# Kernel tuning notes

Measured on AMD Instinct MI355X. Metric: run time of the kernel, lower is better.

Reference implementation:

```python
import jax, jax.numpy as jnp
import numpy as np

HIDDEN = 256
N_HEADS = 4
HEAD_DIM = HIDDEN // N_HEADS
SCALE = float(np.sqrt(HEAD_DIM))


def setup_inputs() -> dict:
    key = jax.random.key(0)
    ks = jax.random.split(key, 10)
    B, NQ, NKV = 2, 4096, 4096
    s = 1.0 / np.sqrt(HIDDEN)
    inp = {
        "query": jax.random.normal(ks[0], (B, NQ, HIDDEN), dtype=jnp.float32),
        "key_value": jax.random.normal(ks[1], (B, NKV, HIDDEN), dtype=jnp.float32),
        "kv_mask": jnp.ones((B, NKV), dtype=jnp.int32),
        "Wq": jax.random.uniform(ks[2], (HIDDEN, HIDDEN), jnp.float32, -s, s),
        "bq": jnp.zeros((HIDDEN,), jnp.float32),
        "Wk": jax.random.uniform(ks[3], (HIDDEN, HIDDEN), jnp.float32, -s, s),
        "bk": jnp.zeros((HIDDEN,), jnp.float32),
        "Wv": jax.random.uniform(ks[4], (HIDDEN, HIDDEN), jnp.float32, -s, s),
        "bv": jnp.zeros((HIDDEN,), jnp.float32),
        "Wo": jax.random.uniform(ks[5], (HIDDEN, HIDDEN), jnp.float32, -s, s),
        "bo": jnp.zeros((HIDDEN,), jnp.float32),
    }
    return inp


def reference(query, key_value, kv_mask, Wq, bq, Wk, bk, Wv, bv, Wo, bo):
    B, NQ, D = query.shape
    NKV = key_value.shape[1]
    # projections; reshape to (B, H, S, Dh)
    q = (query @ Wq + bq).reshape(B, NQ, N_HEADS, HEAD_DIM).transpose(0, 2, 1, 3)
    k = (key_value @ Wk + bk).reshape(B, NKV, N_HEADS, HEAD_DIM).transpose(0, 2, 1, 3)
    v = (key_value @ Wv + bv).reshape(B, NKV, N_HEADS, HEAD_DIM).transpose(0, 2, 1, 3)
    # scores: (B, H, NQ, NKV)
    attn = jnp.einsum("bhqd,bhkd->bhqk", q, k) / SCALE
    mask = (kv_mask != 0)[:, None, None, :]  # (B,1,1,NKV)
    attn = jnp.where(mask, attn, -jnp.inf)
    attn = jax.nn.softmax(attn, axis=-1)
    # dropout is identity in eval mode (reference is deterministic)
    out = jnp.einsum("bhqk,bhkd->bhqd", attn, v)
    out = out.transpose(0, 2, 1, 3).reshape(B, NQ, D)
    return out @ Wo + bo
```

## Files before the change

kernel.cpp:

```cpp
#include <hip/hip_runtime.h>
#include <hip/hip_bf16.h>
#include <math.h>

#define HID   256
#define NHEADS  4
#define HDIM   64
#define SEQ  4096
#define BATCH   2
#define MTOK (BATCH * SEQ)
#define LOG2E 1.44269504088896340736f
#define MFIX  8.0f

typedef short bf16x8 __attribute__((ext_vector_type(8)));
typedef float f32x4  __attribute__((ext_vector_type(4)));

__device__ __forceinline__ unsigned short f2b(float f) {
  union { float f; unsigned u; } v; v.f = f;
  return (unsigned short)((v.u + 0x7FFFu + ((v.u >> 16) & 1u)) >> 16);
}
__device__ __forceinline__ unsigned pkb(float a, float b) {
  __hip_bfloat162 h = __float22bfloat162_rn(make_float2(a, b));
  union { __hip_bfloat162 h; unsigned u; } v; v.h = h;
  return v.u;
}
__device__ __forceinline__ float exp2_(float x) {
#if __has_builtin(__builtin_amdgcn_exp2f)
  return __builtin_amdgcn_exp2f(x);
#else
  return exp2f(x);
#endif
}

__global__ __launch_bounds__(256)
void cast_wt(const float* __restrict__ W0, const float* __restrict__ W1,
             const float* __restrict__ W2, const float* __restrict__ W3,
             unsigned short* __restrict__ Wt) {
  __shared__ float t[64][65];
  const float* Ws[4] = {W0, W1, W2, W3};
  const float scl[4] = {0.125f * LOG2E, 1.f, 1.f, 1.f};
  const int wsel = blockIdx.y;
  const float* W = Ws[wsel];
  const float s = scl[wsel];
  unsigned short* O = Wt + (size_t)wsel * HID * HID;
  const int kt = (blockIdx.x & 3) * 64, nt = (blockIdx.x >> 2) * 64;
  const int tid = threadIdx.x;
#pragma unroll
  for (int p = 0; p < 4; ++p) {
    int i = p * 256 + tid;
    int r = i >> 4, c4 = (i & 15) * 4;
    *(float4*)&t[r][c4] = *(const float4*)&W[(size_t)(kt + r) * HID + nt + c4];
  }
  __syncthreads();
#pragma unroll
  for (int p = 0; p < 4; ++p) {
    int i = p * 256 + tid;
    int rn = i >> 4, ck = (i & 15) * 4;
    ushort4 o;
    o.x = f2b(t[ck + 0][rn] * s);
    o.y = f2b(t[ck + 1][rn] * s);
    o.z = f2b(t[ck + 2][rn] * s);
    o.w = f2b(t[ck + 3][rn] * s);
    *(ushort4*)&O[(size_t)(nt + rn) * HID + kt + ck] = o;
  }
}

__global__ __launch_bounds__(256)
void gemm_qkv(const float* __restrict__ query, const float* __restrict__ keyv,
              const unsigned short* __restrict__ wts,
              const float* __restrict__ bq, const float* __restrict__ bk,
              const float* __restrict__ bv,
              unsigned short* qp, unsigned short* kp, unsigned short* vtp) {
  __shared__ __align__(16) unsigned short As[2][64][136];
  __shared__ __align__(16) unsigned short Bs[64][136];
  float (*L)[68] = (float (*)[68])&Bs[0][0];

  const int tid = threadIdx.x;
  const int w = tid >> 6, lane = tid & 63, lq = lane & 15, quad = lane >> 4;
  const int wm = w & 1, wn = w >> 1;
  const int z = blockIdx.y;
  const int m0 = blockIdx.x * 64;

  const float* A = (z == 0) ? query : keyv;
  const unsigned short* Bt = wts + (size_t)z * HID * HID;
  const float* bias = (z == 0) ? bq : ((z == 1) ? bk : bv);
  const float bscale = (z == 0) ? 0.125f * LOG2E : 1.0f;

#pragma unroll
  for (int p = 0; p < 16; ++p) {
    int i = p * 256 + tid;
    int r = i >> 6, c4 = (i & 63) * 4;
    float4 f4 = *(const float4*)&A[(size_t)(m0 + r) * HID + c4];
    unsigned lo = pkb(f4.x, f4.y), hi = pkb(f4.z, f4.w);
    *(uint2*)&As[c4 >> 7][r][c4 & 127] = make_uint2(lo, hi);
  }
  __syncthreads();

  for (int n = 0; n < 4; ++n) {
    const int n0 = n * 64;
    f32x4 acc[2][2];
#pragma unroll
    for (int i = 0; i < 2; ++i)
#pragma unroll
      for (int j = 0; j < 2; ++j) acc[i][j] = (f32x4){0.f, 0.f, 0.f, 0.f};

#pragma unroll
    for (int kt = 0; kt < 2; ++kt) {
#pragma unroll
      for (int p = 0; p < 4; ++p) {
        int i = p * 256 + tid;
        int r = i >> 4, c8 = (i & 15) * 8;
        *(uint4*)&Bs[r][c8] =
            *(const uint4*)&Bt[(size_t)(n0 + r) * HID + kt * 128 + c8];
      }
      __syncthreads();
#pragma unroll
      for (int ks = 0; ks < 4; ++ks) {
        bf16x8 a0 = *(const bf16x8*)&As[kt][wm * 32 + lq][ks * 32 + quad * 8];
        bf16x8 a1 = *(const bf16x8*)&As[kt][wm * 32 + 16 + lq][ks * 32 + quad * 8];
        bf16x8 b0 = *(const bf16x8*)&Bs[wn * 32 + lq][ks * 32 + quad * 8];
        bf16x8 b1 = *(const bf16x8*)&Bs[wn * 32 + 16 + lq][ks * 32 + quad * 8];
        acc[0][0] = __builtin_amdgcn_mfma_f32_16x16x32_bf16(a0, b0, acc[0][0], 0, 0, 0);
        acc[0][1] = __builtin_amdgcn_mfma_f32_16x16x32_bf16(a0, b1, acc[0][1], 0, 0, 0);
        acc[1][0] = __builtin_amdgcn_mfma_f32_16x16x32_bf16(a1, b0, acc[1][0], 0, 0, 0);
        acc[1][1] = __builtin_amdgcn_mfma_f32_16x16x32_bf16(a1, b1, acc[1][1], 0, 0, 0);
      }
      __syncthreads();
    }

#pragma unroll
    for (int ni = 0; ni < 2; ++ni) {
      const float bv = bias[n0 + wn * 32 + ni * 16 + lq] * bscale;
#pragma unroll
      for (int mi = 0; mi < 2; ++mi)
#pragma unroll
        for (int r = 0; r < 4; ++r)
          L[wm * 32 + mi * 16 + quad * 4 + r][wn * 32 + ni * 16 + lq] =
              acc[mi][ni][r] + bv;
    }
    __syncthreads();

    if (z == 2) {
      const int nn = tid >> 2, mb4 = (tid & 3) * 16;
      __align__(16) unsigned short tmp[16];
#pragma unroll
      for (int j = 0; j < 16; ++j) {
        int p = mb4 + j;
        int k = ((p & 3) << 4) + (p >> 2);
        tmp[j] = f2b(L[k][nn]);
      }
      *(uint4*)&vtp[(size_t)(n0 + nn) * MTOK + m0 + mb4]     = *(uint4*)&tmp[0];
      *(uint4*)&vtp[(size_t)(n0 + nn) * MTOK + m0 + mb4 + 8] = *(uint4*)&tmp[8];
    } else {
      unsigned short* Y = (z == 0) ? qp : kp;
      const int r = tid >> 2, cb = (tid & 3) * 16;
      __align__(16) unsigned short tmp[16];
#pragma unroll
      for (int j = 0; j < 4; ++j) {
        float4 v4 = *(const float4*)&L[r][cb + j * 4];
        *(uint2*)&tmp[j * 4] = make_uint2(pkb(v4.x, v4.y), pkb(v4.z, v4.w));
      }
      *(uint4*)&Y[(size_t)(m0 + r) * HID + n0 + cb]     = *(uint4*)&tmp[0];
      *(uint4*)&Y[(size_t)(m0 + r) * HID + n0 + cb + 8] = *(uint4*)&tmp[8];
    }
    __syncthreads();
  }
}

__global__ __launch_bounds__(256)
void gemm_out(const unsigned short* __restrict__ ao,
              const unsigned short* __restrict__ wot,
              const float* __restrict__ bo, float* __restrict__ out) {
  __shared__ __align__(16) unsigned short As[64][136];
  __shared__ __align__(16) unsigned short Bs[64][136];
  float (*L)[68] = (float (*)[68])&As[0][0];

  const int tid = threadIdx.x;
  const int w = tid >> 6, lane = tid & 63, lq = lane & 15, quad = lane >> 4;
  const int wm = w & 1, wn = w >> 1;
  const int m0 = blockIdx.y * 64, n0 = blockIdx.x * 64;

  f32x4 acc[2][2];
#pragma unroll
  for (int i = 0; i < 2; ++i)
#pragma unroll
    for (int j = 0; j < 2; ++j) acc[i][j] = (f32x4){0.f, 0.f, 0.f, 0.f};

#pragma unroll
  for (int kt = 0; kt < 2; ++kt) {
    const int k0 = kt * 128;
#pragma unroll
    for (int p = 0; p < 4; ++p) {
      int i = p * 256 + tid;
      int r = i >> 4, c8 = (i & 15) * 8;
      *(uint4*)&As[r][c8] = *(const uint4*)&ao[(size_t)(m0 + r) * HID + k0 + c8];
      *(uint4*)&Bs[r][c8] = *(const uint4*)&wot[(size_t)(n0 + r) * HID + k0 + c8];
    }
    __syncthreads();
#pragma unroll
    for (int ks = 0; ks < 4; ++ks) {
      bf16x8 a0 = *(const bf16x8*)&As[wm * 32 + lq][ks * 32 + quad * 8];
      bf16x8 a1 = *(const bf16x8*)&As[wm * 32 + 16 + lq][ks * 32 + quad * 8];
      bf16x8 b0 = *(const bf16x8*)&Bs[wn * 32 + lq][ks * 32 + quad * 8];
      bf16x8 b1 = *(const bf16x8*)&Bs[wn * 32 + 16 + lq][ks * 32 + quad * 8];
      acc[0][0] = __builtin_amdgcn_mfma_f32_16x16x32_bf16(a0, b0, acc[0][0], 0, 0, 0);
      acc[0][1] = __builtin_amdgcn_mfma_f32_16x16x32_bf16(a0, b1, acc[0][1], 0, 0, 0);
      acc[1][0] = __builtin_amdgcn_mfma_f32_16x16x32_bf16(a1, b0, acc[1][0], 0, 0, 0);
      acc[1][1] = __builtin_amdgcn_mfma_f32_16x16x32_bf16(a1, b1, acc[1][1], 0, 0, 0);
    }
    __syncthreads();
  }

#pragma unroll
  for (int ni = 0; ni < 2; ++ni) {
    const float bv = bo[n0 + wn * 32 + ni * 16 + lq];
#pragma unroll
    for (int mi = 0; mi < 2; ++mi)
#pragma unroll
      for (int r = 0; r < 4; ++r)
        L[wm * 32 + mi * 16 + quad * 4 + r][wn * 32 + ni * 16 + lq] =
            acc[mi][ni][r] + bv;
  }
  __syncthreads();

  const int r = tid >> 2, cb = (tid & 3) * 16;
#pragma unroll
  for (int j = 0; j < 4; ++j) {
    float4 v4 = *(const float4*)&L[r][cb + j * 4];
    *(float4*)&out[(size_t)(m0 + r) * HID + n0 + cb + j * 4] = v4;
  }
}

__global__ __launch_bounds__(512, 1)
void flash_attn_mfma(const unsigned short* __restrict__ Qp,
                     const unsigned short* __restrict__ Kp,
                     const unsigned short* __restrict__ Vtp,
                     const int* __restrict__ mask,
                     unsigned short* __restrict__ Ao) {
  __shared__ __align__(16) unsigned short Ks[2][128][72];
  __shared__ __align__(16) unsigned short Vt[2][64][136];
  __shared__ __align__(16) unsigned short Ps[8][16][72];
  __shared__ float mb[2][128];

  const int tid = threadIdx.x;
  const int w = tid >> 6, lane = tid & 63, lq = lane & 15, quad = lane >> 4;
  const int bh = blockIdx.x;
  const int b = bh >> 2, h = bh & 3;
  const int q0 = blockIdx.y * 128;
  const int qbase = b * SEQ + q0, kvbase = b * SEQ, coff = h * HDIM;

  const int rk0 = tid >> 3,          ck0 = (tid & 7) * 8;
  const int rk1 = (512 + tid) >> 3,  ck1 = ((512 + tid) & 7) * 8;
  const int rv0 = tid >> 4,          cv0 = (tid & 15) * 8;
  const int rv1 = (512 + tid) >> 4,  cv1 = ((512 + tid) & 15) * 8;

  bf16x8 qf0, qf1;
  {
    const unsigned short* qr = &Qp[(size_t)(qbase + w * 16 + lq) * HID + coff + quad * 8];
    qf0 = *(const bf16x8*)&qr[0];
    qf1 = *(const bf16x8*)&qr[32];
  }

  const short oneb = (short)0x3F80;
  const bf16x8 ones = {oneb, oneb, oneb, oneb, oneb, oneb, oneb, oneb};

  f32x4 o[4], ls;
#pragma unroll
  for (int c = 0; c < 4; ++c) o[c] = (f32x4){0.f, 0.f, 0.f, 0.f};
  ls = (f32x4){0.f, 0.f, 0.f, 0.f};

  {
    *(uint4*)&Ks[0][rk0][ck0] =
        *(const uint4*)&Kp[(size_t)(kvbase + rk0) * HID + coff + ck0];
    *(uint4*)&Ks[0][rk1][ck1] =
        *(const uint4*)&Kp[(size_t)(kvbase + rk1) * HID + coff + ck1];
    *(uint4*)&Vt[0][rv0][cv0] =
        *(const uint4*)&Vtp[(size_t)(coff + rv0) * MTOK + kvbase + cv0];
    *(uint4*)&Vt[0][rv1][cv1] =
        *(const uint4*)&Vtp[(size_t)(coff + rv1) * MTOK + kvbase + cv1];
    if (tid < 128) mb[0][tid] = mask[kvbase + tid] ? -MFIX : -1e30f;
  }
  __syncthreads();

  const int NT = SEQ / 128;
  for (int t = 0; t < NT; ++t) {
    const int cur = t & 1, nxt = cur ^ 1;
    const bool pf = (t + 1 < NT);

    uint4 kA, kB, vA, vB;
    float mbr = 0.f;
    if (pf) {
      const int k0n = (t + 1) * 128;
      kA = *(const uint4*)&Kp[(size_t)(kvbase + k0n + rk0) * HID + coff + ck0];
      kB = *(const uint4*)&Kp[(size_t)(kvbase + k0n + rk1) * HID + coff + ck1];
      vA = *(const uint4*)&Vtp[(size_t)(coff + rv0) * MTOK + kvbase + k0n + cv0];
      vB = *(const uint4*)&Vtp[(size_t)(coff + rv1) * MTOK + kvbase + k0n + cv1];
      if (tid < 128) mbr = mask[kvbase + k0n + tid] ? -MFIX : -1e30f;
    }

    f32x4 sc[8];
#pragma unroll
    for (int c = 0; c < 8; ++c) {
      sc[c] = (f32x4){0.f, 0.f, 0.f, 0.f};
      bf16x8 kb0 = *(const bf16x8*)&Ks[cur][c * 16 + lq][quad * 8];
      bf16x8 kb1 = *(const bf16x8*)&Ks[cur][c * 16 + lq][32 + quad * 8];
      sc[c] = __builtin_amdgcn_mfma_f32_16x16x32_bf16(qf0, kb0, sc[c], 0, 0, 0);
      sc[c] = __builtin_amdgcn_mfma_f32_16x16x32_bf16(qf1, kb1, sc[c], 0, 0, 0);
    }
    float mbias[8];
#pragma unroll
    for (int c = 0; c < 8; ++c) mbias[c] = mb[cur][c * 16 + lq];

#pragma unroll
    for (int hh = 0; hh < 2; ++hh) {
#pragma unroll
      for (int r = 0; r < 4; ++r) {
        const int row = quad * 4 + r;
        unsigned a0 = pkb(exp2_(sc[hh * 4 + 0][r] + mbias[hh * 4 + 0]),
                          exp2_(sc[hh * 4 + 1][r] + mbias[hh * 4 + 1]));
        unsigned a1 = pkb(exp2_(sc[hh * 4 + 2][r] + mbias[hh * 4 + 2]),
                          exp2_(sc[hh * 4 + 3][r] + mbias[hh * 4 + 3]));
        *(uint2*)&Ps[w][row][lq * 4] = make_uint2(a0, a1);
      }
#pragma unroll
      for (int i = 0; i < 2; ++i) {
        bf16x8 pa = *(const bf16x8*)&Ps[w][lq][i * 32 + quad * 8];
        ls = __builtin_amdgcn_mfma_f32_16x16x32_bf16(pa, ones, ls, 0, 0, 0);
#pragma unroll
        for (int c = 0; c < 4; ++c) {
          bf16x8 vb = *(const bf16x8*)&Vt[cur][c * 16 + lq][hh * 64 + i * 32 + quad * 8];
          o[c] = __builtin_amdgcn_mfma_f32_16x16x32_bf16(pa, vb, o[c], 0, 0, 0);
        }
      }
    }

    if (pf) {
      *(uint4*)&Ks[nxt][rk0][ck0] = kA;
      *(uint4*)&Ks[nxt][rk1][ck1] = kB;
      *(uint4*)&Vt[nxt][rv0][cv0] = vA;
      *(uint4*)&Vt[nxt][rv1][cv1] = vB;
      if (tid < 128) mb[nxt][tid] = mbr;
    }
    __syncthreads();
  }

#pragma unroll
  for (int r = 0; r < 4; ++r) {
    float inv = 1.f / ls[r];
    const size_t row = (size_t)(qbase + w * 16 + quad * 4 + r);
#pragma unroll
    for (int c = 0; c < 4; ++c)
      Ao[row * HID + coff + c * 16 + lq] = f2b(o[c][r] * inv);
  }
}

extern "C" void kernel_launch(void* const* d_in, const int* in_sizes, int n_in,
                              void* d_out, int out_size, void* d_ws, size_t ws_size,
                              hipStream_t stream) {
  const float* query = (const float*)d_in[0];
  const float* keyv  = (const float*)d_in[1];
  const int*   mask  = (const int*)d_in[2];
  const float* Wq = (const float*)d_in[3];
  const float* bq = (const float*)d_in[4];
  const float* Wk = (const float*)d_in[5];
  const float* bk = (const float*)d_in[6];
  const float* Wv = (const float*)d_in[7];
  const float* bv = (const float*)d_in[8];
  const float* Wo = (const float*)d_in[9];
  const float* bo = (const float*)d_in[10];
  float* out = (float*)d_out;

  unsigned short* wts = (unsigned short*)d_ws;
  unsigned short* qp  = wts + (size_t)4 * HID * HID;
  unsigned short* kp  = qp  + (size_t)MTOK * HID;
  unsigned short* vtp = kp  + (size_t)MTOK * HID;
  unsigned short* ao  = vtp + (size_t)MTOK * HID;

  const unsigned short* wo_t = wts + 3 * HID * HID;

  dim3 blk(256);
  hipLaunchKernelGGL(cast_wt, dim3(16, 4), blk, 0, stream, Wq, Wk, Wv, Wo, wts);

  dim3 qkvgrid(MTOK / 64, 3);
  hipLaunchKernelGGL(gemm_qkv, qkvgrid, blk, 0, stream,
                     query, keyv, wts, bq, bk, bv, qp, kp, vtp);

  dim3 fgrid(BATCH * NHEADS, SEQ / 128);
  hipLaunchKernelGGL(flash_attn_mfma, fgrid, dim3(512), 0, stream,
                     qp, kp, vtp, mask, ao);

  dim3 ogrid(HID / 64, MTOK / 64);
  hipLaunchKernelGGL(gemm_out, ogrid, blk, 0, stream, ao, wo_t, bo, out);
}
```

Measured before the change: 161.5 us.

## Split attention warps into 2x2 query/key groups with LDS reduction of partial outputs

Each warp now handles 32 query rows against half of the 128-key tile, instead of 16 query rows against the whole tile. Every K and V fragment read from LDS then feeds two MFMAs, which halves LDS fragment traffic per FLOP. The two key-group partial outputs and row sums are combined at the end through shared memory reused from the enlarged P buffer. The cost is more accumulator registers per warp, an extra sync, and the final reduction.

New measurement: 159.5 us. About the same (-1.2%).

```diff
diff --git a/kernel.cpp b/kernel.cpp
--- a/kernel.cpp
+++ b/kernel.cpp
@@ -238,11 +238,15 @@
                      unsigned short* __restrict__ Ao) {
   __shared__ __align__(16) unsigned short Ks[2][128][72];
   __shared__ __align__(16) unsigned short Vt[2][64][136];
-  __shared__ __align__(16) unsigned short Ps[8][16][72];
+  __shared__ __align__(16) unsigned short Ps[8][32][72];
   __shared__ float mb[2][128];
+
+  float (*Ored)[32][68] = (float (*)[32][68])&Ps[0][0][0];
+  float* Lred = (float*)((char*)&Ps[0][0][0] + sizeof(float) * 4 * 32 * 68);
 
   const int tid = threadIdx.x;
   const int w = tid >> 6, lane = tid & 63, lq = lane & 15, quad = lane >> 4;
+  const int qg = w >> 1, kg = w & 1;
   const int bh = blockIdx.x;
   const int b = bh >> 2, h = bh & 3;
   const int q0 = blockIdx.y * 128;
@@ -253,20 +257,25 @@
   const int rv0 = tid >> 4,          cv0 = (tid & 15) * 8;
   const int rv1 = (512 + tid) >> 4,  cv1 = ((512 + tid) & 15) * 8;
 
-  bf16x8 qf0, qf1;
-  {
-    const unsigned short* qr = &Qp[(size_t)(qbase + w * 16 + lq) * HID + coff + quad * 8];
-    qf0 = *(const bf16x8*)&qr[0];
-    qf1 = *(const bf16x8*)&qr[32];
+  bf16x8 qf[2][2];
+#pragma unroll
+  for (int m = 0; m < 2; ++m) {
+    const unsigned short* qr =
+        &Qp[(size_t)(qbase + qg * 32 + m * 16 + lq) * HID + coff + quad * 8];
+    qf[m][0] = *(const bf16x8*)&qr[0];
+    qf[m][1] = *(const bf16x8*)&qr[32];
   }
 
   const short oneb = (short)0x3F80;
   const bf16x8 ones = {oneb, oneb, oneb, oneb, oneb, oneb, oneb, oneb};
 
-  f32x4 o[4], ls;
-#pragma unroll
-  for (int c = 0; c < 4; ++c) o[c] = (f32x4){0.f, 0.f, 0.f, 0.f};
-  ls = (f32x4){0.f, 0.f, 0.f, 0.f};
+  f32x4 o[2][4], ls2[2];
+#pragma unroll
+  for (int m = 0; m < 2; ++m) {
+    ls2[m] = (f32x4){0.f, 0.f, 0.f, 0.f};
+#pragma unroll
+    for (int dc = 0; dc < 4; ++dc) o[m][dc] = (f32x4){0.f, 0.f, 0.f, 0.f};
+  }
 
   {
     *(uint4*)&Ks[0][rk0][ck0] =
@@ -297,39 +306,49 @@
       if (tid < 128) mbr = mask[kvbase + k0n + tid] ? -MFIX : -1e30f;
     }
 
-    f32x4 sc[8];
-#pragma unroll
-    for (int c = 0; c < 8; ++c) {
-      sc[c] = (f32x4){0.f, 0.f, 0.f, 0.f};
-      bf16x8 kb0 = *(const bf16x8*)&Ks[cur][c * 16 + lq][quad * 8];
-      bf16x8 kb1 = *(const bf16x8*)&Ks[cur][c * 16 + lq][32 + quad * 8];
-      sc[c] = __builtin_amdgcn_mfma_f32_16x16x32_bf16(qf0, kb0, sc[c], 0, 0, 0);
-      sc[c] = __builtin_amdgcn_mfma_f32_16x16x32_bf16(qf1, kb1, sc[c], 0, 0, 0);
-    }
-    float mbias[8];
-#pragma unroll
-    for (int c = 0; c < 8; ++c) mbias[c] = mb[cur][c * 16 + lq];
-
-#pragma unroll
-    for (int hh = 0; hh < 2; ++hh) {
+    f32x4 sc[2][4];
+#pragma unroll
+    for (int m = 0; m < 2; ++m)
+#pragma unroll
+      for (int c = 0; c < 4; ++c) sc[m][c] = (f32x4){0.f, 0.f, 0.f, 0.f};
+#pragma unroll
+    for (int c = 0; c < 4; ++c) {
+      bf16x8 kb0 = *(const bf16x8*)&Ks[cur][kg * 64 + c * 16 + lq][quad * 8];
+      bf16x8 kb1 = *(const bf16x8*)&Ks[cur][kg * 64 + c * 16 + lq][32 + quad * 8];
+      sc[0][c] = __builtin_amdgcn_mfma_f32_16x16x32_bf16(qf[0][0], kb0, sc[0][c], 0, 0, 0);
+      sc[0][c] = __builtin_amdgcn_mfma_f32_16x16x32_bf16(qf[0][1], kb1, sc[0][c], 0, 0, 0);
+      sc[1][c] = __builtin_amdgcn_mfma_f32_16x16x32_bf16(qf[1][0], kb0, sc[1][c], 0, 0, 0);
+      sc[1][c] = __builtin_amdgcn_mfma_f32_16x16x32_bf16(qf[1][1], kb1, sc[1][c], 0, 0, 0);
+    }
+    float mbias[4];
+#pragma unroll
+    for (int c = 0; c < 4; ++c) mbias[c] = mb[cur][kg * 64 + c * 16 + lq];
+
+#pragma unroll
+    for (int m = 0; m < 2; ++m) {
 #pragma unroll
       for (int r = 0; r < 4; ++r) {
-        const int row = quad * 4 + r;
-        unsigned a0 = pkb(exp2_(sc[hh * 4 + 0][r] + mbias[hh * 4 + 0]),
-                          exp2_(sc[hh * 4 + 1][r] + mbias[hh * 4 + 1]));
-        unsigned a1 = pkb(exp2_(sc[hh * 4 + 2][r] + mbias[hh * 4 + 2]),
-                          exp2_(sc[hh * 4 + 3][r] + mbias[hh * 4 + 3]));
+        const int row = m * 16 + quad * 4 + r;
+        unsigned a0 = pkb(exp2_(sc[m][0][r] + mbias[0]),
+                          exp2_(sc[m][1][r] + mbias[1]));
+        unsigned a1 = pkb(exp2_(sc[m][2][r] + mbias[2]),
+                          exp2_(sc[m][3][r] + mbias[3]));
         *(uint2*)&Ps[w][row][lq * 4] = make_uint2(a0, a1);
       }
-#pragma unroll
-      for (int i = 0; i < 2; ++i) {
-        bf16x8 pa = *(const bf16x8*)&Ps[w][lq][i * 32 + quad * 8];
-        ls = __builtin_amdgcn_mfma_f32_16x16x32_bf16(pa, ones, ls, 0, 0, 0);
-#pragma unroll
-        for (int c = 0; c < 4; ++c) {
-          bf16x8 vb = *(const bf16x8*)&Vt[cur][c * 16 + lq][hh * 64 + i * 32 + quad * 8];
-          o[c] = __builtin_amdgcn_mfma_f32_16x16x32_bf16(pa, vb, o[c], 0, 0, 0);
-        }
+    }
+
+#pragma unroll
+    for (int i = 0; i < 2; ++i) {
+      bf16x8 pa0 = *(const bf16x8*)&Ps[w][lq][i * 32 + quad * 8];
+      bf16x8 pa1 = *(const bf16x8*)&Ps[w][16 + lq][i * 32 + quad * 8];
+      ls2[0] = __builtin_amdgcn_mfma_f32_16x16x32_bf16(pa0, ones, ls2[0], 0, 0, 0);
+      ls2[1] = __builtin_amdgcn_mfma_f32_16x16x32_bf16(pa1, ones, ls2[1], 0, 0, 0);
+#pragma unroll
+      for (int dc = 0; dc < 4; ++dc) {
+        bf16x8 vb =
+            *(const bf16x8*)&Vt[cur][dc * 16 + lq][kg * 64 + i * 32 + quad * 8];
+        o[0][dc] = __builtin_amdgcn_mfma_f32_16x16x32_bf16(pa0, vb, o[0][dc], 0, 0, 0);
+        o[1][dc] = __builtin_amdgcn_mfma_f32_16x16x32_bf16(pa1, vb, o[1][dc], 0, 0, 0);
       }
     }
 
@@ -343,13 +362,36 @@
     __syncthreads();
   }
 
-#pragma unroll
-  for (int r = 0; r < 4; ++r) {
-    float inv = 1.f / ls[r];
-    const size_t row = (size_t)(qbase + w * 16 + quad * 4 + r);
-#pragma unroll
-    for (int c = 0; c < 4; ++c)
-      Ao[row * HID + coff + c * 16 + lq] = f2b(o[c][r] * inv);
+  if (kg == 1) {
+#pragma unroll
+    for (int m = 0; m < 2; ++m) {
+#pragma unroll
+      for (int r = 0; r < 4; ++r) {
+        const int row = m * 16 + quad * 4 + r;
+        if (lq == 0) Lred[qg * 32 + row] = ls2[m][r];
+#pragma unroll
+        for (int dc = 0; dc < 4; ++dc)
+          Ored[qg][row][dc * 16 + lq] = o[m][dc][r];
+      }
+    }
+  }
+  __syncthreads();
+  if (kg == 0) {
+#pragma unroll
+    for (int m = 0; m < 2; ++m) {
+#pragma unroll
+      for (int r = 0; r < 4; ++r) {
+        const int row = m * 16 + quad * 4 + r;
+        const float l = ls2[m][r] + Lred[qg * 32 + row];
+        const float inv = 1.f / l;
+        const size_t grow = (size_t)(qbase + qg * 32 + row);
+#pragma unroll
+        for (int dc = 0; dc < 4; ++dc) {
+          const float val = (o[m][dc][r] + Ored[qg][row][dc * 16 + lq]) * inv;
+          Ao[grow * HID + coff + dc * 16 + lq] = f2b(val);
+        }
+      }
+    }
   }
 }
 
```
